# Kernel tuning notes

Measured on AMD Instinct MI355X. Metric: run time of the kernel, lower is better.

The kernel has to match this reference:

```python
import jax, jax.numpy as jnp
import numpy as np

HEADS = 16


def fenwick_mask(T):
    # Boolean [T, T] mask: diagonal + Fenwick-tree lookback positions, causal.
    m = np.zeros((T, T), dtype=bool)
    for i in range(T):
        j = i + 1
        while j <= T:
            m[i, j - 1] = True
            j += j & -j
        step = 1
        while i - step >= 0:
            m[i, i - step] = True
            step *= 2
    m &= np.tril(np.ones((T, T), dtype=bool))  # causal
    return jnp.asarray(m)


def setup_inputs() -> dict:
    key = jax.random.key(0)
    ks = jax.random.split(key, 4)
    B, T, C = 2, 2048, 1024
    x = jax.random.normal(ks[0], (B, T, C), dtype=jnp.float32)
    W_qkv = jax.random.normal(ks[1], (C, 3 * C), dtype=jnp.float32) * (C ** -0.5)
    b_qkv = jnp.zeros((3 * C,), dtype=jnp.float32)
    W_proj = jax.random.normal(ks[2], (C, C), dtype=jnp.float32) * (C ** -0.5)
    b_proj = jnp.zeros((C,), dtype=jnp.float32)
    return {"x": x, "W_qkv": W_qkv, "b_qkv": b_qkv, "W_proj": W_proj, "b_proj": b_proj}


def reference(x, W_qkv, b_qkv, W_proj, b_proj):
    B, T, C = x.shape
    H = HEADS
    Dh = C // H
    scale = Dh ** -0.5
    qkv = (x @ W_qkv + b_qkv).reshape(B, T, 3, H, Dh)
    qkv = jnp.transpose(qkv, (2, 0, 3, 1, 4))  # [3, B, H, T, Dh]
    q, k, v = qkv[0], qkv[1], qkv[2]
    attn = jnp.einsum('bhtd,bhsd->bhts', q, k) * scale  # [B, H, T, T]
    mask = fenwick_mask(T)  # trace-time constant
    attn = jnp.where(mask[None, None], attn, -jnp.inf)
    attn = jax.nn.softmax(attn, axis=-1)
    out = jnp.einsum('bhts,bhsd->bhtd', attn, v)  # [B, H, T, Dh]
    out = jnp.transpose(out, (0, 2, 1, 3)).reshape(B, T, C)
    return out @ W_proj + b_proj
```

## Files before the change

### kernel.cpp

```cpp
#include <hip/hip_runtime.h>
#include <hip/hip_bf16.h>


typedef unsigned short ushort_t;
typedef __attribute__((ext_vector_type(8))) short s16x8;
typedef __attribute__((ext_vector_type(4))) float f32x4;

#define T_SEQ 2048
#define C_DIM 1024
#define HEADS 16

__device__ __forceinline__ ushort_t f2bf(float f) {
    union { float f; unsigned u; } v{f};
    unsigned r = v.u + 0x7FFFu + ((v.u >> 16) & 1u);
    return (ushort_t)(r >> 16);
}
__device__ __forceinline__ float bf2f(ushort_t u) {
    union { unsigned u; float f; } v{((unsigned)u) << 16};
    return v.f;
}

__device__ __forceinline__ void async16(const ushort_t* g, ushort_t* l) {
    __builtin_amdgcn_global_load_lds(
        (const __attribute__((address_space(1))) void*)g,
        (__attribute__((address_space(3))) void*)l, 16, 0, 0);
}

__global__ void prep(const float* __restrict__ x, ushort_t* __restrict__ xb,
                     const float* __restrict__ Wq, ushort_t* __restrict__ WqT,
                     const float* __restrict__ Wp, ushort_t* __restrict__ WpT) {
    const int bid = blockIdx.x;
    const int tid = threadIdx.x;
    if (bid < 4096) {
        const int i = bid * 256 + tid;
        float4 f = ((const float4*)x)[i];
        ushort4 o;
        o.x = f2bf(f.x); o.y = f2bf(f.y); o.z = f2bf(f.z); o.w = f2bf(f.w);
        ((ushort4*)xb)[i] = o;
    } else {
        __shared__ ushort_t tile[32][33];
        const float* W; ushort_t* WT; int N, nb, kb;
        if (bid < 7168) {
            const int tb = bid - 4096;
            W = Wq; WT = WqT; N = 3072; nb = (tb % 96) * 32; kb = (tb / 96) * 32;
        } else {
            const int tb = bid - 7168;
            W = Wp; WT = WpT; N = 1024; nb = (tb & 31) * 32; kb = (tb >> 5) * 32;
        }
        const int tx = tid & 31, ty = tid >> 5;
        #pragma unroll
        for (int i = ty; i < 32; i += 8)
            tile[i][tx] = f2bf(W[(size_t)(kb + i) * N + nb + tx]);
        __syncthreads();
        #pragma unroll
        for (int i = ty; i < 32; i += 8)
            WT[(size_t)(nb + i) * 1024 + kb + tx] = tile[tx][i];
    }
}


#define BAR()  do { __builtin_amdgcn_sched_barrier(0); __builtin_amdgcn_s_barrier(); \
                    __builtin_amdgcn_sched_barrier(0); } while (0)
#define WAIT_LGKM0() do { asm volatile("s_waitcnt lgkmcnt(0)" ::: "memory"); \
                          __builtin_amdgcn_sched_barrier(0); } while (0)
#define WAIT_VM(n)  asm volatile("s_waitcnt vmcnt(" #n ")" ::: "memory")

#define SA(kt, u, dst) async16(Ag + (size_t)(u) * rstep + (size_t)(kt) * 64, \
                               (dst) + (u) * 4096 + wave * 512)
#define SB(kt, u, dst) async16(Bg + (size_t)(u) * rstep + (size_t)(kt) * 64, \
                               (dst) + (u) * 4096 + wave * 512)

#define LDA_FRAG(buf, i, kh) (*(const s16x8*)((buf) + ((wm << 7) + (i) * 16 + lrow) * 64 \
                               + ((((kh) * 4 + quad) ^ d3) << 3)))
#define LDB_FRAG(buf, j, kh) (*(const s16x8*)((buf) + (wn * 48 + (j) * 16 + lrow) * 64 \
                               + ((((kh) * 4 + quad) ^ d3) << 3)))

#define PHASE(lAb, lBb, Q, LOADB, STAGES, ENDWAIT)                              \
  {                                                                             \
    s16x8 af[2][2];                                                             \
    _Pragma("unroll") for (int ii = 0; ii < 2; ++ii)                            \
      _Pragma("unroll") for (int kh = 0; kh < 2; ++kh)                          \
        af[ii][kh] = LDA_FRAG(lAb, 2 * (Q) + ii, kh);                           \
    if (LOADB) {                                                                \
      _Pragma("unroll") for (int j = 0; j < 3; ++j)                             \
        _Pragma("unroll") for (int kh = 0; kh < 2; ++kh)                        \
          bf[j][kh] = LDB_FRAG(lBb, j, kh);                                     \
    }                                                                           \
    STAGES;                                                                     \
    BAR();                                                                      \
    WAIT_LGKM0();                                                               \
    __builtin_amdgcn_s_setprio(1);                                              \
    _Pragma("unroll") for (int ii = 0; ii < 2; ++ii)                            \
      _Pragma("unroll") for (int j = 0; j < 3; ++j)                             \
        _Pragma("unroll") for (int kh = 0; kh < 2; ++kh)                        \
          acc[2 * (Q) + ii][j] = __builtin_amdgcn_mfma_f32_16x16x32_bf16(       \
              af[ii][kh], bf[j][kh], acc[2 * (Q) + ii][j], 0, 0, 0);            \
    __builtin_amdgcn_s_setprio(0);                                              \
    ENDWAIT;                                                                    \
    BAR();                                                                      \
  }

__global__ __launch_bounds__(512, 2)
void gemm_qkv(const ushort_t* __restrict__ A, const ushort_t* __restrict__ BT,
              const float* __restrict__ bias, ushort_t* __restrict__ C,
              int N, int K) {
    __shared__ ushort_t lds[57344];

    const int tid  = threadIdx.x;
    const int wave = tid >> 6;
    const int lane = tid & 63;
    const int wm   = wave >> 2;
    const int wn   = wave & 3;
    const int lrow = lane & 15;
    const int quad = lane >> 4;
    const int d3   = lrow & 7;
    const int crow = lane >> 3;
    const int gcol = (((lane & 7) ^ crow) << 3);
    const int row0 = blockIdx.x * 256;
    const int col0 = blockIdx.y * 192;

    ushort_t* const lA0 = lds;
    ushort_t* const lB0 = lds + 16384;
    ushort_t* const lA1 = lds + 28672;
    ushort_t* const lB1 = lds + 45056;

    const ushort_t* Ag = A  + (size_t)(row0 + wave * 8 + crow) * K + gcol;
    const ushort_t* Bg = BT + (size_t)(col0 + wave * 8 + crow) * K + gcol;
    const size_t rstep = (size_t)64 * K;

    f32x4 acc[8][3] = {};
    s16x8 bf[3][2];

    SA(0, 0, lA0); SA(0, 1, lA0); SA(0, 2, lA0); SA(0, 3, lA0);
    SB(0, 0, lB0); SB(0, 1, lB0); SB(0, 2, lB0);
    SB(1, 0, lB1); SB(1, 1, lB1); SA(1, 0, lA1); SA(1, 2, lA1); SB(1, 2, lB1);
    WAIT_VM(5);
    BAR();

    const int nt = K >> 6;
    for (int t = 0; t < nt; t += 2) {
        const bool s2 = (t + 2) < nt;
        const bool s3 = (t + 3) < nt;
        PHASE(lA0, lB0, 0, true,  { SA(t + 1, 1, lA1); SA(t + 1, 3, lA1); }, {});
        PHASE(lA0, lB0, 1, false, { if (s2) { SB(t + 2, 0, lB0); SB(t + 2, 1, lB0); } }, {});
        PHASE(lA0, lB0, 2, false, { if (s2) { SA(t + 2, 0, lA0); SA(t + 2, 2, lA0); } }, {});
        PHASE(lA0, lB0, 3, false, { if (s2) { SB(t + 2, 2, lB0); } },
              { if (s2) { WAIT_VM(5); } else { WAIT_VM(0); } });
        PHASE(lA1, lB1, 0, true,  { if (s2) { SA(t + 2, 1, lA0); SA(t + 2, 3, lA0); } }, {});
        PHASE(lA1, lB1, 1, false, { if (s3) { SB(t + 3, 0, lB1); SB(t + 3, 1, lB1); } }, {});
        PHASE(lA1, lB1, 2, false, { if (s3) { SA(t + 3, 0, lA1); SA(t + 3, 2, lA1); } }, {});
        PHASE(lA1, lB1, 3, false, { if (s3) { SB(t + 3, 2, lB1); } },
              { WAIT_VM(5); });
    }

    #pragma unroll
    for (int i = 0; i < 8; ++i) {
        #pragma unroll
        for (int j = 0; j < 3; ++j) {
            const int col = col0 + wn * 48 + j * 16 + lrow;
            const float bv = bias[col];
            #pragma unroll
            for (int r = 0; r < 4; ++r) {
                const int row = row0 + (wm << 7) + i * 16 + quad * 4 + r;
                C[(size_t)row * N + col] = f2bf(acc[i][j][r] + bv);
            }
        }
    }
}

__global__ void gemm_proj(const ushort_t* __restrict__ A, const ushort_t* __restrict__ BT,
                          const float* __restrict__ bias, float* __restrict__ C,
                          int N, int K) {
    __shared__ ushort_t lsA[128 * 64];
    __shared__ ushort_t lsB[64 * 64];

    const int tid  = threadIdx.x;
    const int wave = tid >> 6;
    const int lane = tid & 63;
    const int row0 = blockIdx.x * 128;
    const int col0 = blockIdx.y * 64;
    const int lrow = lane & 15;
    const int quad = lane >> 4;
    const int crow = lane >> 3;
    const int gcol = ((lane & 7) ^ crow) * 8;
    const int d3   = lrow & 7;

    f32x4 acc[2][4] = {};

    for (int k0 = 0; k0 < K; k0 += 64) {
        #pragma unroll
        for (int it = 0; it < 4; ++it) {
            const int chunk = it * 4 + wave;
            const int r = chunk * 8 + crow;
            async16(A + (size_t)(row0 + r) * K + (k0 + gcol), lsA + chunk * 512);
        }
        #pragma unroll
        for (int it = 0; it < 2; ++it) {
            const int chunk = it * 4 + wave;
            const int r = chunk * 8 + crow;
            async16(BT + (size_t)(col0 + r) * K + (k0 + gcol), lsB + chunk * 512);
        }
        __syncthreads();
        #pragma unroll
        for (int kk = 0; kk < 64; kk += 32) {
            const int g = (kk >> 3) + quad;
            const int slot = (g ^ d3) << 3;
            s16x8 af[2], bfr[4];
            #pragma unroll
            for (int i = 0; i < 2; ++i)
                af[i] = *(const s16x8*)(lsA + (wave * 32 + i * 16 + lrow) * 64 + slot);
            #pragma unroll
            for (int j = 0; j < 4; ++j)
                bfr[j] = *(const s16x8*)(lsB + (j * 16 + lrow) * 64 + slot);
            #pragma unroll
            for (int i = 0; i < 2; ++i)
                #pragma unroll
                for (int j = 0; j < 4; ++j)
                    acc[i][j] = __builtin_amdgcn_mfma_f32_16x16x32_bf16(
                        af[i], bfr[j], acc[i][j], 0, 0, 0);
        }
        __syncthreads();
    }

    #pragma unroll
    for (int i = 0; i < 2; ++i) {
        #pragma unroll
        for (int j = 0; j < 4; ++j) {
            const int col = col0 + j * 16 + lrow;
            const float bv = bias[col];
            #pragma unroll
            for (int r = 0; r < 4; ++r) {
                const int row = row0 + wave * 32 + i * 16 + quad * 4 + r;
                C[(size_t)row * N + col] = acc[i][j][r] + bv;
            }
        }
    }
}

__global__ void fenwick_attn(const ushort_t* __restrict__ QKV, ushort_t* __restrict__ AO) {
    const int lane = threadIdx.x & 63;
    const int wid  = blockIdx.x * 4 + (threadIdx.x >> 6);
    const int tile = wid & 255;
    const int bh   = wid >> 8;
    const int h    = bh & (HEADS - 1);
    const int b    = bh >> 4;
    const int tl   = lane >> 3;
    const int g    = lane & 7;
    const int t    = tile * 8 + tl;

    const ushort_t* base = QKV + (size_t)(b * T_SEQ) * 3072 + h * 64 + g * 8;

    float qf[8];
    {
        s16x8 qv = *(const s16x8*)(base + (size_t)t * 3072);
        #pragma unroll
        for (int e = 0; e < 8; ++e) qf[e] = bf2f((ushort_t)qv[e]);
    }

    float logit[12];
    int   pos[12];
    float mx = -1e30f;
    #pragma unroll
    for (int s = 0; s < 12; ++s) {
        const int step = (s == 0) ? 0 : (1 << (s - 1));
        const bool act = (step <= t);
        const int p = act ? (t - step) : t;
        pos[s] = p;
        s16x8 kv = *(const s16x8*)(base + (size_t)p * 3072 + 1024);
        float l = 0.f;
        #pragma unroll
        for (int e = 0; e < 8; ++e) l = fmaf(qf[e], bf2f((ushort_t)kv[e]), l);
        l += __shfl_xor(l, 1, 64);
        l += __shfl_xor(l, 2, 64);
        l += __shfl_xor(l, 4, 64);
        l *= 0.125f;
        logit[s] = act ? l : -1e30f;
        mx = fmaxf(mx, logit[s]);
    }

    float denom = 0.f;
    float ov[8] = {};
    #pragma unroll
    for (int s = 0; s < 12; ++s) {
        const float w = __expf(logit[s] - mx);
        denom += w;
        s16x8 vv = *(const s16x8*)(base + (size_t)pos[s] * 3072 + 2048);
        #pragma unroll
        for (int e = 0; e < 8; ++e) ov[e] = fmaf(w, bf2f((ushort_t)vv[e]), ov[e]);
    }

    const float inv = 1.f / denom;
    s16x8 os;
    #pragma unroll
    for (int e = 0; e < 8; ++e) os[e] = (short)f2bf(ov[e] * inv);
    *(s16x8*)(AO + (size_t)(b * T_SEQ + t) * C_DIM + h * 64 + g * 8) = os;
}

extern "C" void kernel_launch(void* const* d_in, const int* in_sizes, int n_in,
                              void* d_out, int out_size, void* d_ws, size_t ws_size,
                              hipStream_t stream) {
    const float* x      = (const float*)d_in[0];
    const float* W_qkv  = (const float*)d_in[1];
    const float* b_qkv  = (const float*)d_in[2];
    const float* W_proj = (const float*)d_in[3];
    const float* b_proj = (const float*)d_in[4];
    float* out = (float*)d_out;

    char* ws = (char*)d_ws;
    ushort_t* xb     = (ushort_t*)(ws);
    ushort_t* WqkvT  = (ushort_t*)(ws + (size_t)8  * 1048576);
    ushort_t* QKVb   = (ushort_t*)(ws + (size_t)14 * 1048576);
    ushort_t* AO     = (ushort_t*)(ws + (size_t)38 * 1048576);
    ushort_t* WprojT = (ushort_t*)(ws + (size_t)46 * 1048576);

    prep<<<8192, 256, 0, stream>>>(x, xb, W_qkv, WqkvT, W_proj, WprojT);
    gemm_qkv<<<dim3(16, 16), 512, 0, stream>>>(xb, WqkvT, b_qkv, QKVb, 3072, 1024);
    fenwick_attn<<<2048, 256, 0, stream>>>(QKVb, AO);
    gemm_proj<<<dim3(32, 16), 256, 0, stream>>>(AO, WprojT, b_proj, out, 1024, 1024);
}
```

Measured before the change: 149.2 us.

## Remap blocks per XCD for L2 locality and enlarge proj GEMM tiles

Replaces 2D grids with 1D grids whose block ids are remapped so that blocks landing on the same XCD (bid&7) share row/column panels of A and B, or the same batch-head in attention, to improve L2 reuse. The output-projection GEMM goes from 128x64 to 128x128 tiles per block, with each wave computing a 64x64 sub-tile. This doubles reuse of loaded A data and halves the grid to 256 blocks. The cost is more registers and LDS per block and fewer blocks to hide latency.

```diff
diff --git a/kernel.cpp b/kernel.cpp
--- a/kernel.cpp
+++ b/kernel.cpp
@@ -57,7 +57,6 @@
             WT[(size_t)(nb + i) * 1024 + kb + tx] = tile[tx][i];
     }
 }
-
 
 #define BAR()  do { __builtin_amdgcn_sched_barrier(0); __builtin_amdgcn_s_barrier(); \
                     __builtin_amdgcn_sched_barrier(0); } while (0)
@@ -116,8 +115,14 @@
     const int d3   = lrow & 7;
     const int crow = lane >> 3;
     const int gcol = (((lane & 7) ^ crow) << 3);
-    const int row0 = blockIdx.x * 256;
-    const int col0 = blockIdx.y * 192;
+
+    const int bid    = blockIdx.x;
+    const int xcd    = bid & 7;
+    const int q      = bid >> 3;
+    const int rowblk = ((xcd & 3) << 2) + (q & 3);
+    const int colblk = ((xcd >> 2) << 3) + (q >> 2);
+    const int row0   = rowblk * 256;
+    const int col0   = colblk * 192;
 
     ushort_t* const lA0 = lds;
     ushort_t* const lB0 = lds + 16384;
@@ -172,32 +177,34 @@
                           const float* __restrict__ bias, float* __restrict__ C,
                           int N, int K) {
     __shared__ ushort_t lsA[128 * 64];
-    __shared__ ushort_t lsB[64 * 64];
+    __shared__ ushort_t lsB[128 * 64];
 
     const int tid  = threadIdx.x;
     const int wave = tid >> 6;
     const int lane = tid & 63;
-    const int row0 = blockIdx.x * 128;
-    const int col0 = blockIdx.y * 64;
+
+    const int bid  = blockIdx.x;
+    const int xcd  = bid & 7;
+    const int q    = bid >> 3;
+    const int row0 = (xcd * 4 + (q & 3)) * 128;
+    const int col0 = (q >> 2) * 128;
+
+    const int wr   = (wave >> 1) * 64;
+    const int wc   = (wave & 1) * 64;
     const int lrow = lane & 15;
     const int quad = lane >> 4;
     const int crow = lane >> 3;
     const int gcol = ((lane & 7) ^ crow) * 8;
     const int d3   = lrow & 7;
 
-    f32x4 acc[2][4] = {};
+    f32x4 acc[4][4] = {};
 
     for (int k0 = 0; k0 < K; k0 += 64) {
         #pragma unroll
         for (int it = 0; it < 4; ++it) {
             const int chunk = it * 4 + wave;
             const int r = chunk * 8 + crow;
-            async16(A + (size_t)(row0 + r) * K + (k0 + gcol), lsA + chunk * 512);
-        }
-        #pragma unroll
-        for (int it = 0; it < 2; ++it) {
-            const int chunk = it * 4 + wave;
-            const int r = chunk * 8 + crow;
+            async16(A  + (size_t)(row0 + r) * K + (k0 + gcol), lsA + chunk * 512);
             async16(BT + (size_t)(col0 + r) * K + (k0 + gcol), lsB + chunk * 512);
         }
         __syncthreads();
@@ -205,15 +212,15 @@
         for (int kk = 0; kk < 64; kk += 32) {
             const int g = (kk >> 3) + quad;
             const int slot = (g ^ d3) << 3;
-            s16x8 af[2], bfr[4];
-            #pragma unroll
-            for (int i = 0; i < 2; ++i)
-                af[i] = *(const s16x8*)(lsA + (wave * 32 + i * 16 + lrow) * 64 + slot);
+            s16x8 af[4], bfr[4];
+            #pragma unroll
+            for (int i = 0; i < 4; ++i)
+                af[i] = *(const s16x8*)(lsA + (wr + i * 16 + lrow) * 64 + slot);
             #pragma unroll
             for (int j = 0; j < 4; ++j)
-                bfr[j] = *(const s16x8*)(lsB + (j * 16 + lrow) * 64 + slot);
-            #pragma unroll
-            for (int i = 0; i < 2; ++i)
+                bfr[j] = *(const s16x8*)(lsB + (wc + j * 16 + lrow) * 64 + slot);
+            #pragma unroll
+            for (int i = 0; i < 4; ++i)
                 #pragma unroll
                 for (int j = 0; j < 4; ++j)
                     acc[i][j] = __builtin_amdgcn_mfma_f32_16x16x32_bf16(
@@ -223,14 +230,14 @@
     }
 
     #pragma unroll
-    for (int i = 0; i < 2; ++i) {
+    for (int i = 0; i < 4; ++i) {
         #pragma unroll
         for (int j = 0; j < 4; ++j) {
-            const int col = col0 + j * 16 + lrow;
+            const int col = col0 + wc + j * 16 + lrow;
             const float bv = bias[col];
             #pragma unroll
             for (int r = 0; r < 4; ++r) {
-                const int row = row0 + wave * 32 + i * 16 + quad * 4 + r;
+                const int row = row0 + wr + i * 16 + quad * 4 + r;
                 C[(size_t)row * N + col] = acc[i][j][r] + bv;
             }
         }
@@ -239,9 +246,11 @@
 
 __global__ void fenwick_attn(const ushort_t* __restrict__ QKV, ushort_t* __restrict__ AO) {
     const int lane = threadIdx.x & 63;
-    const int wid  = blockIdx.x * 4 + (threadIdx.x >> 6);
-    const int tile = wid & 255;
-    const int bh   = wid >> 8;
+    const int bid  = blockIdx.x;
+    const int xcd  = bid & 7;
+    const int q    = bid >> 3;
+    const int bh   = xcd + ((q >> 6) << 3);
+    const int tile = ((q & 63) << 2) + (threadIdx.x >> 6);
     const int h    = bh & (HEADS - 1);
     const int b    = bh >> 4;
     const int tl   = lane >> 3;
@@ -314,7 +323,7 @@
     ushort_t* WprojT = (ushort_t*)(ws + (size_t)46 * 1048576);
 
     prep<<<8192, 256, 0, stream>>>(x, xb, W_qkv, WqkvT, W_proj, WprojT);
-    gemm_qkv<<<dim3(16, 16), 512, 0, stream>>>(xb, WqkvT, b_qkv, QKVb, 3072, 1024);
+    gemm_qkv<<<256, 512, 0, stream>>>(xb, WqkvT, b_qkv, QKVb, 3072, 1024);
     fenwick_attn<<<2048, 256, 0, stream>>>(QKVb, AO);
-    gemm_proj<<<dim3(32, 16), 256, 0, stream>>>(AO, WprojT, b_proj, out, 1024, 1024);
-}
+    gemm_proj<<<256, 256, 0, stream>>>(AO, WprojT, b_proj, out, 1024, 1024);
+}
```

Measured after the change: 148.1 us. No clear change (-0.7%).
